# Kernel optimization log

Measured on AMD Instinct MI355X. Metric: run time of the kernel, lower is better.

## Reference

```python
import jax, jax.numpy as jnp
import numpy as np

B, IN_DIM, MEM = 8192, 4096, 256
MIN_TS, MAX_TS, EPS = 0.1, 10.0, 1e-6
LN_EPS = 1e-5


def setup_inputs() -> dict:
    key = jax.random.key(0)
    ks = jax.random.split(key, 10)
    std = 0.02
    d_in = MEM + IN_DIM  # 4352
    return {
        "x": jax.random.normal(ks[0], (B, IN_DIM), jnp.float32),
        "h": jax.random.normal(ks[1], (B, MEM), jnp.float32),
        # memory_target: Linear(d_in, 2*MEM) -> LN -> GELU -> Linear(2*MEM, MEM)
        "W1": std * jax.random.normal(ks[2], (d_in, 2 * MEM), jnp.float32),
        "b1": jnp.zeros((2 * MEM,), jnp.float32),
        "g1": jnp.ones((2 * MEM,), jnp.float32),
        "be1": jnp.zeros((2 * MEM,), jnp.float32),
        "W2": std * jax.random.normal(ks[3], (2 * MEM, MEM), jnp.float32),
        "b2": jnp.zeros((MEM,), jnp.float32),
        # decay_gate: Linear(d_in, MEM) -> sigmoid
        "Wd": std * jax.random.normal(ks[4], (d_in, MEM), jnp.float32),
        "bd": jnp.zeros((MEM,), jnp.float32),
        # input_gate: Linear(d_in, MEM) -> sigmoid
        "Wu": std * jax.random.normal(ks[5], (d_in, MEM), jnp.float32),
        "bu": jnp.zeros((MEM,), jnp.float32),
    }


def _layernorm(t, g, b):
    mu = jnp.mean(t, axis=-1, keepdims=True)
    var = jnp.mean(jnp.square(t - mu), axis=-1, keepdims=True)
    return (t - mu) * jax.lax.rsqrt(var + LN_EPS) * g + b


def reference(x, h, W1, b1, g1, be1, W2, b2, Wd, bd, Wu, bu):
    combined = jnp.concatenate([h, x], axis=-1)  # [B, MEM+IN_DIM]
    # memory_target branch: Linear -> LayerNorm -> GELU (exact) -> Linear -> tanh
    t = _layernorm(combined @ W1 + b1, g1, be1)
    t = jax.nn.gelu(t, approximate=False)
    h_candidate = jnp.tanh(t @ W2 + b2)  # [B, MEM]
    # gates
    decay = jax.nn.sigmoid(combined @ Wd + bd)
    update = jax.nn.sigmoid(combined @ Wu + bu)
    decay = MIN_TS + (MAX_TS - MIN_TS) * decay + EPS
    new_h = (1.0 - update) * (h / decay) + update * h_candidate
    # normalize_memory: rescale new_h to old h's L2 norm
    h_norm = jnp.maximum(jnp.linalg.norm(h, axis=-1, keepdims=True), EPS)
    nh_norm = jnp.maximum(jnp.linalg.norm(new_h, axis=-1, keepdims=True), 1e-12)
    new_h = new_h / nh_norm * h_norm
    return new_h
```

## Files before the change

kernel.cpp:

```cpp
#include <hip/hip_runtime.h>
#include <stdint.h>

typedef unsigned short u16;

#define B_ROWS 8192
#define IN_DIM 4096
#define MEM 256
#define D_IN 4352
#define N1 1024
#define K2 512
#define LN_EPS 1e-5f

typedef __attribute__((ext_vector_type(4))) float f32x4;
typedef __attribute__((ext_vector_type(4))) uint32_t u32x4;
typedef __attribute__((ext_vector_type(4))) unsigned short u16x4;
typedef __attribute__((ext_vector_type(8))) short bf16x8;

#define AS1(p) ((__attribute__((address_space(1))) void*)(p))
#define AS3(p) ((__attribute__((address_space(3))) void*)(p))

__device__ __forceinline__ float bf2f(u16 u) {
  union { uint32_t u; float f; } c; c.u = ((uint32_t)u) << 16; return c.f;
}
__device__ __forceinline__ u16 f2bf(float f) {
  union { float f; uint32_t u; } c; c.f = f;
  uint32_t r = (c.u + 0x7fffu + ((c.u >> 16) & 1u)) >> 16;
  return (u16)r;
}
__device__ __forceinline__ uint32_t fbits(float f) {
  union { float f; uint32_t u; } c; c.f = f; return c.u;
}
__device__ __forceinline__ uint32_t pack_trunc(float a, float b) {
  return (fbits(b) & 0xFFFF0000u) | (fbits(a) >> 16);
}

__global__ __launch_bounds__(256)
void transpose_cast_fused(const float* __restrict__ W1, const float* __restrict__ Wd,
                          const float* __restrict__ Wu, u16* __restrict__ WT) {
  __shared__ u16 tile[64][68];
  int n0 = blockIdx.x * 64, k0 = blockIdx.y * 64;
  const float* src; int srcN, ns0;
  if (n0 < 512)      { src = W1; srcN = 512; ns0 = n0; }
  else if (n0 < 768) { src = Wd; srcN = 256; ns0 = n0 - 512; }
  else               { src = Wu; srcN = 256; ns0 = n0 - 768; }
  int t = threadIdx.x;
  int rr = t >> 4;
  int c4 = (t & 15) * 4;
#pragma unroll
  for (int i = 0; i < 4; i++) {
    int k = i * 16 + rr;
    f32x4 v = *(const f32x4*)&src[(size_t)(k0 + k) * srcN + ns0 + c4];
    tile[c4 + 0][k] = f2bf(v[0]);
    tile[c4 + 1][k] = f2bf(v[1]);
    tile[c4 + 2][k] = f2bf(v[2]);
    tile[c4 + 3][k] = f2bf(v[3]);
  }
  __syncthreads();
#pragma unroll
  for (int i = 0; i < 4; i++) {
    int n = i * 16 + rr;
    u16x4 w;
    w.x = tile[n][c4 + 0];
    w.y = tile[n][c4 + 1];
    w.z = tile[n][c4 + 2];
    w.w = tile[n][c4 + 3];
    *(u16x4*)&WT[(size_t)(n0 + n) * D_IN + k0 + c4] = w;
  }
}

__global__ void transpose_cast(const float* __restrict__ src, u16* __restrict__ dst,
                               int K, int N) {
  __shared__ u16 tile[32][34];
  int n0 = blockIdx.x * 32, k0 = blockIdx.y * 32;
  int tx = threadIdx.x, ty = threadIdx.y;
#pragma unroll
  for (int i = 0; i < 4; i++)
    tile[ty + i * 8][tx] = f2bf(src[(size_t)(k0 + ty + i * 8) * N + n0 + tx]);
  __syncthreads();
#pragma unroll
  for (int i = 0; i < 4; i++)
    dst[(size_t)(n0 + ty + i * 8) * K + k0 + tx] = tile[tx][ty + i * 8];
}

__global__ __launch_bounds__(256, 4)
void gemm1_kernel(const float* __restrict__ x, const float* __restrict__ h,
                  const u16* __restrict__ WT, u16* __restrict__ G0,
                  u16* __restrict__ G1, int klen) {
  __shared__ __attribute__((aligned(16))) u16 As[128 * 64];
  __shared__ __attribute__((aligned(16))) u16 Bs[128 * 64];
  const int t = threadIdx.x;
  const int lane = t & 63, wave = t >> 6;
  const int by = blockIdx.x & 63;
  const int bx = (blockIdx.x >> 6) & 7;
  const int part = blockIdx.x >> 9;
  const int kbase = part * klen;
  u16* __restrict__ Gout = part ? G1 : G0;
  const int row0 = by * 128, col0 = bx * 128;
  const int q = lane >> 4, mrow = lane & 15;
  const int wm = wave >> 1, wn = wave & 1;

  int ar[4], ac[4];
#pragma unroll
  for (int j = 0; j < 4; j++) {
    int idx = j * 256 + t;
    int r = idx >> 3;
    ar[j] = r;
    ac[j] = (idx & 7) ^ (r & 7);
  }

  f32x4 acc[4][4] = {};

  for (int k0 = kbase; k0 < kbase + klen; k0 += 64) {
#pragma unroll
    for (int j = 0; j < 4; j++) {
      const u16* gp = WT + (size_t)(col0 + ar[j]) * D_IN + k0 + ac[j] * 8;
      __builtin_amdgcn_global_load_lds(AS1(gp), AS3(&Bs[(j * 256 + t) * 8]), 16, 0, 0);
    }
#pragma unroll
    for (int j = 0; j < 4; j++) {
      int k = k0 + ac[j] * 8;
      const float* gp = (k < MEM) ? (h + (size_t)(row0 + ar[j]) * MEM + k)
                                  : (x + (size_t)(row0 + ar[j]) * IN_DIM + (k - MEM));
      f32x4 v0 = *(const f32x4*)gp;
      f32x4 v1 = *(const f32x4*)(gp + 4);
      u32x4 w;
      w.x = pack_trunc(v0[0], v0[1]);
      w.y = pack_trunc(v0[2], v0[3]);
      w.z = pack_trunc(v1[0], v1[1]);
      w.w = pack_trunc(v1[2], v1[3]);
      *(u32x4*)&As[(j * 256 + t) * 8] = w;
    }
    __syncthreads();
#pragma unroll
    for (int kk = 0; kk < 2; kk++) {
      bf16x8 a[4], b[4];
#pragma unroll
      for (int mt = 0; mt < 4; mt++) {
        int row = wm * 64 + mt * 16 + mrow;
        int p = (kk * 4 + q) ^ (mrow & 7);
        a[mt] = *(const bf16x8*)&As[row * 64 + p * 8];
      }
#pragma unroll
      for (int nt = 0; nt < 4; nt++) {
        int row = wn * 64 + nt * 16 + mrow;
        int p = (kk * 4 + q) ^ (mrow & 7);
        b[nt] = *(const bf16x8*)&Bs[row * 64 + p * 8];
      }
#pragma unroll
      for (int mt = 0; mt < 4; mt++) {
#pragma unroll
        for (int nt = 0; nt < 4; nt++) {
          acc[mt][nt] = __builtin_amdgcn_mfma_f32_16x16x32_bf16(a[mt], b[nt], acc[mt][nt], 0, 0, 0);
        }
      }
    }
    __syncthreads();
  }
#pragma unroll
  for (int mt = 0; mt < 4; mt++) {
#pragma unroll
    for (int nt = 0; nt < 4; nt++) {
#pragma unroll
      for (int i = 0; i < 4; i++) {
        int row = row0 + wm * 64 + mt * 16 + q * 4 + i;
        int col = col0 + wn * 64 + nt * 16 + mrow;
        Gout[(size_t)row * N1 + col] = f2bf(acc[mt][nt][i]);
      }
    }
  }
}

__global__ __launch_bounds__(256)
void ln_gelu_kernel(u16* __restrict__ G0, const u16* __restrict__ G1,
                    const float* __restrict__ b1, const float* __restrict__ g1,
                    const float* __restrict__ be1, int nparts) {
  int r = blockIdx.x;
  int t = threadIdx.x;
  u16* row = G0 + (size_t)r * N1;
  uint32_t w = *(const uint32_t*)&row[2 * t];
  float z0 = bf2f((u16)(w & 0xffff));
  float z1 = bf2f((u16)(w >> 16));
  if (nparts == 2) {
    uint32_t w1 = *(const uint32_t*)&G1[(size_t)r * N1 + 2 * t];
    z0 += bf2f((u16)(w1 & 0xffff));
    z1 += bf2f((u16)(w1 >> 16));
  }
  z0 += b1[2 * t];
  z1 += b1[2 * t + 1];
  float s = z0 + z1, ss = z0 * z0 + z1 * z1;
#pragma unroll
  for (int m = 32; m >= 1; m >>= 1) {
    s += __shfl_xor(s, m, 64);
    ss += __shfl_xor(ss, m, 64);
  }
  __shared__ float rs[4], rss[4];
  int lane = t & 63, wave = t >> 6;
  if (lane == 0) { rs[wave] = s; rss[wave] = ss; }
  __syncthreads();
  float S = rs[0] + rs[1] + rs[2] + rs[3];
  float SS = rss[0] + rss[1] + rss[2] + rss[3];
  float mu = S * (1.0f / 512.0f);
  float var = SS * (1.0f / 512.0f) - mu * mu;
  float rstd = rsqrtf(var + LN_EPS);
  float y0 = (z0 - mu) * rstd * g1[2 * t] + be1[2 * t];
  float y1 = (z1 - mu) * rstd * g1[2 * t + 1] + be1[2 * t + 1];
  float o0 = 0.5f * y0 * (1.0f + erff(y0 * 0.7071067811865475f));
  float o1 = 0.5f * y1 * (1.0f + erff(y1 * 0.7071067811865475f));
  *(uint32_t*)&row[2 * t] = ((uint32_t)f2bf(o1) << 16) | f2bf(o0);
}

__global__ __launch_bounds__(256, 2)
void gemm2_epi_kernel(const u16* __restrict__ G0, const u16* __restrict__ G1,
                      const u16* __restrict__ W2T, const float* __restrict__ h,
                      const float* __restrict__ b2, const float* __restrict__ bd,
                      const float* __restrict__ bu, float* __restrict__ out,
                      int nparts) {
  __shared__ __attribute__((aligned(16))) u16 As[32 * 64];
  __shared__ __attribute__((aligned(16))) u16 Bs[256 * 64];
  __shared__ float red_nh[32][4], red_h[32][4], scl[32];
  const int t = threadIdx.x, lane = t & 63, wave = t >> 6;
  const int q = lane >> 4, mrow = lane & 15;
  const int r0 = blockIdx.x * 32;

  const int arA = t >> 3;
  const int acA = (t & 7) ^ (arA & 7);
  int brB[8], bcB[8];
#pragma unroll
  for (int j = 0; j < 8; j++) {
    int idx = j * 256 + t;
    brB[j] = idx >> 3;
    bcB[j] = (idx & 7) ^ (brB[j] & 7);
  }
  f32x4 acc[2][4] = {};
  for (int k0 = 0; k0 < K2; k0 += 64) {
    __builtin_amdgcn_global_load_lds(AS1(G0 + (size_t)(r0 + arA) * N1 + k0 + acA * 8),
                                     AS3(&As[t * 8]), 16, 0, 0);
#pragma unroll
    for (int j = 0; j < 8; j++) {
      __builtin_amdgcn_global_load_lds(AS1(W2T + (size_t)brB[j] * K2 + k0 + bcB[j] * 8),
                                       AS3(&Bs[(j * 256 + t) * 8]), 16, 0, 0);
    }
    __syncthreads();
#pragma unroll
    for (int kk = 0; kk < 2; kk++) {
      bf16x8 a[2], b[4];
#pragma unroll
      for (int mt = 0; mt < 2; mt++) {
        int row = mt * 16 + mrow;
        int p = (kk * 4 + q) ^ (row & 7);
        a[mt] = *(const bf16x8*)&As[row * 64 + p * 8];
      }
#pragma unroll
      for (int nt = 0; nt < 4; nt++) {
        int row = wave * 64 + nt * 16 + mrow;
        int p = (kk * 4 + q) ^ (row & 7);
        b[nt] = *(const bf16x8*)&Bs[row * 64 + p * 8];
      }
#pragma unroll
      for (int mt = 0; mt < 2; mt++) {
#pragma unroll
        for (int nt = 0; nt < 4; nt++) {
          acc[mt][nt] = __builtin_amdgcn_mfma_f32_16x16x32_bf16(a[mt], b[nt], acc[mt][nt], 0, 0, 0);
        }
      }
    }
    __syncthreads();
  }
  float snh[2][4], shh[2][4];
#pragma unroll
  for (int mt = 0; mt < 2; mt++) {
#pragma unroll
    for (int i = 0; i < 4; i++) {
      int r = mt * 16 + q * 4 + i;
      size_t grow = (size_t)(r0 + r);
      float a_nh = 0.f, a_h = 0.f;
#pragma unroll
      for (int nt = 0; nt < 4; nt++) {
        int c = wave * 64 + nt * 16 + mrow;
        float hc = tanhf(acc[mt][nt][i] + b2[c]);
        float zd = bf2f(G0[grow * N1 + 512 + c]);
        float zu = bf2f(G0[grow * N1 + 768 + c]);
        if (nparts == 2) {
          zd += bf2f(G1[grow * N1 + 512 + c]);
          zu += bf2f(G1[grow * N1 + 768 + c]);
        }
        zd += bd[c];
        zu += bu[c];
        float dec = 0.1f + 9.9f / (1.0f + expf(-zd)) + 1e-6f;
        float u = 1.0f / (1.0f + expf(-zu));
        float hv = h[grow * MEM + c];
        float nh = (1.0f - u) * (hv / dec) + u * hc;
        acc[mt][nt][i] = nh;
        a_nh += nh * nh;
        a_h += hv * hv;
      }
      snh[mt][i] = a_nh;
      shh[mt][i] = a_h;
    }
  }
#pragma unroll
  for (int m = 1; m <= 8; m <<= 1) {
#pragma unroll
    for (int mt = 0; mt < 2; mt++) {
#pragma unroll
      for (int i = 0; i < 4; i++) {
        snh[mt][i] += __shfl_xor(snh[mt][i], m, 64);
        shh[mt][i] += __shfl_xor(shh[mt][i], m, 64);
      }
    }
  }
  if (mrow == 0) {
#pragma unroll
    for (int mt = 0; mt < 2; mt++) {
#pragma unroll
      for (int i = 0; i < 4; i++) {
        int r = mt * 16 + q * 4 + i;
        red_nh[r][wave] = snh[mt][i];
        red_h[r][wave] = shh[mt][i];
      }
    }
  }
  __syncthreads();
  if (t < 32) {
    float tn = red_nh[t][0] + red_nh[t][1] + red_nh[t][2] + red_nh[t][3];
    float th = red_h[t][0] + red_h[t][1] + red_h[t][2] + red_h[t][3];
    float hn = fmaxf(sqrtf(th), 1e-6f);
    float nn = fmaxf(sqrtf(tn), 1e-12f);
    scl[t] = hn / nn;
  }
  __syncthreads();
#pragma unroll
  for (int mt = 0; mt < 2; mt++) {
#pragma unroll
    for (int i = 0; i < 4; i++) {
      int r = mt * 16 + q * 4 + i;
      size_t grow = (size_t)(r0 + r);
      float sc = scl[r];
#pragma unroll
      for (int nt = 0; nt < 4; nt++) {
        int c = wave * 64 + nt * 16 + mrow;
        out[grow * MEM + c] = acc[mt][nt][i] * sc;
      }
    }
  }
}

extern "C" void kernel_launch(void* const* d_in, const int* in_sizes, int n_in,
                              void* d_out, int out_size, void* d_ws, size_t ws_size,
                              hipStream_t stream) {
  const float* x   = (const float*)d_in[0];
  const float* h   = (const float*)d_in[1];
  const float* W1  = (const float*)d_in[2];
  const float* b1  = (const float*)d_in[3];
  const float* g1  = (const float*)d_in[4];
  const float* be1 = (const float*)d_in[5];
  const float* W2  = (const float*)d_in[6];
  const float* b2  = (const float*)d_in[7];
  const float* Wd  = (const float*)d_in[8];
  const float* bd  = (const float*)d_in[9];
  const float* Wu  = (const float*)d_in[10];
  const float* bu  = (const float*)d_in[11];
  float* out = (float*)d_out;

  char* ws = (char*)d_ws;
  u16* WT  = (u16*)(ws);
  u16* W2T = (u16*)(ws + 8912896);
  u16* G0  = (u16*)(ws + 9175040);
  u16* G1  = (u16*)(ws + 25952256);

  const int nparts = (ws_size >= 42729472u) ? 2 : 1;
  const int klen = D_IN / nparts;

  transpose_cast_fused<<<dim3(N1 / 64, D_IN / 64), 256, 0, stream>>>(W1, Wd, Wu, WT);
  transpose_cast<<<dim3(256 / 32, 512 / 32), dim3(32, 8), 0, stream>>>(W2, W2T, 512, 256);

  gemm1_kernel<<<512 * nparts, 256, 0, stream>>>(x, h, WT, G0, G1, klen);
  ln_gelu_kernel<<<B_ROWS, 256, 0, stream>>>(G0, G1, b1, g1, be1, nparts);
  gemm2_epi_kernel<<<B_ROWS / 32, 256, 0, stream>>>(G0, G1, W2T, h, b2, bd, bu, out, nparts);
}
```

Baseline: 388.1 us.

## Fuse LayerNorm+GELU into GEMM2 and pre-cast activations to bf16 for GEMM1

Removes the separate LayerNorm/GELU kernel. Its work moves into the prologue of the second GEMM, which now keeps 16 normalized rows in LDS, cutting one round trip of the intermediate through global memory. When the workspace is large enough, it also adds a separate pass that casts x and h to bf16 once with round-to-nearest-even. The first GEMM can then load A tiles asynchronously straight into LDS instead of converting fp32 in its inner loop. The trade-offs are an extra kernel and an extra bf16 copy of the activations, plus smaller row tiles in GEMM2 that reuse each W2 tile less.

After: 343.2 us. 1.13x faster.

```diff
diff --git a/kernel.cpp b/kernel.cpp
--- a/kernel.cpp
+++ b/kernel.cpp
@@ -30,8 +30,33 @@
 __device__ __forceinline__ uint32_t fbits(float f) {
   union { float f; uint32_t u; } c; c.f = f; return c.u;
 }
+__device__ __forceinline__ uint32_t pack_rne(float a, float b) {
+  return ((uint32_t)f2bf(b) << 16) | f2bf(a);
+}
 __device__ __forceinline__ uint32_t pack_trunc(float a, float b) {
   return (fbits(b) & 0xFFFF0000u) | (fbits(a) >> 16);
+}
+
+__global__ __launch_bounds__(256)
+void cast_A_kernel(const float* __restrict__ h, const float* __restrict__ x,
+                   u16* __restrict__ Abf) {
+  int b = blockIdx.x, t = threadIdx.x;
+  const float* src; int r, c, dcol;
+  if (b < 1024) {
+    int g = (b * 256 + t) * 8;
+    src = h + g; r = g >> 8; c = g & 255; dcol = c;
+  } else {
+    int g = ((b - 1024) * 256 + t) * 8;
+    src = x + g; r = g >> 12; c = g & 4095; dcol = MEM + c;
+  }
+  f32x4 v0 = *(const f32x4*)src;
+  f32x4 v1 = *(const f32x4*)(src + 4);
+  u32x4 w;
+  w.x = pack_rne(v0[0], v0[1]);
+  w.y = pack_rne(v0[2], v0[3]);
+  w.z = pack_rne(v1[0], v1[1]);
+  w.w = pack_rne(v1[2], v1[3]);
+  *(u32x4*)&Abf[(size_t)r * D_IN + dcol] = w;
 }
 
 __global__ __launch_bounds__(256)
@@ -83,9 +108,8 @@
 }
 
 __global__ __launch_bounds__(256, 4)
-void gemm1_kernel(const float* __restrict__ x, const float* __restrict__ h,
-                  const u16* __restrict__ WT, u16* __restrict__ G0,
-                  u16* __restrict__ G1, int klen) {
+void gemm1_pre_kernel(const u16* __restrict__ Abf, const u16* __restrict__ WT,
+                      u16* __restrict__ G0, u16* __restrict__ G1, int klen) {
   __shared__ __attribute__((aligned(16))) u16 As[128 * 64];
   __shared__ __attribute__((aligned(16))) u16 Bs[128 * 64];
   const int t = threadIdx.x;
@@ -118,6 +142,83 @@
     }
 #pragma unroll
     for (int j = 0; j < 4; j++) {
+      const u16* gp = Abf + (size_t)(row0 + ar[j]) * D_IN + k0 + ac[j] * 8;
+      __builtin_amdgcn_global_load_lds(AS1(gp), AS3(&As[(j * 256 + t) * 8]), 16, 0, 0);
+    }
+    __syncthreads();
+#pragma unroll
+    for (int kk = 0; kk < 2; kk++) {
+      bf16x8 a[4], b[4];
+#pragma unroll
+      for (int mt = 0; mt < 4; mt++) {
+        int row = wm * 64 + mt * 16 + mrow;
+        int p = (kk * 4 + q) ^ (mrow & 7);
+        a[mt] = *(const bf16x8*)&As[row * 64 + p * 8];
+      }
+#pragma unroll
+      for (int nt = 0; nt < 4; nt++) {
+        int row = wn * 64 + nt * 16 + mrow;
+        int p = (kk * 4 + q) ^ (mrow & 7);
+        b[nt] = *(const bf16x8*)&Bs[row * 64 + p * 8];
+      }
+#pragma unroll
+      for (int mt = 0; mt < 4; mt++) {
+#pragma unroll
+        for (int nt = 0; nt < 4; nt++) {
+          acc[mt][nt] = __builtin_amdgcn_mfma_f32_16x16x32_bf16(a[mt], b[nt], acc[mt][nt], 0, 0, 0);
+        }
+      }
+    }
+    __syncthreads();
+  }
+#pragma unroll
+  for (int mt = 0; mt < 4; mt++) {
+#pragma unroll
+    for (int nt = 0; nt < 4; nt++) {
+#pragma unroll
+      for (int i = 0; i < 4; i++) {
+        int row = row0 + wm * 64 + mt * 16 + q * 4 + i;
+        int col = col0 + wn * 64 + nt * 16 + mrow;
+        Gout[(size_t)row * N1 + col] = f2bf(acc[mt][nt][i]);
+      }
+    }
+  }
+}
+
+__global__ __launch_bounds__(256, 4)
+void gemm1_inline_kernel(const float* __restrict__ x, const float* __restrict__ h,
+                         const u16* __restrict__ WT, u16* __restrict__ G0,
+                         u16* __restrict__ G1, int klen) {
+  __shared__ __attribute__((aligned(16))) u16 As[128 * 64];
+  __shared__ __attribute__((aligned(16))) u16 Bs[128 * 64];
+  const int t = threadIdx.x;
+  const int lane = t & 63, wave = t >> 6;
+  const int by = blockIdx.x & 63;
+  const int bx = (blockIdx.x >> 6) & 7;
+  const int part = blockIdx.x >> 9;
+  const int kbase = part * klen;
+  u16* __restrict__ Gout = part ? G1 : G0;
+  const int row0 = by * 128, col0 = bx * 128;
+  const int q = lane >> 4, mrow = lane & 15;
+  const int wm = wave >> 1, wn = wave & 1;
+
+  int ar[4], ac[4];
+#pragma unroll
+  for (int j = 0; j < 4; j++) {
+    int idx = j * 256 + t;
+    int r = idx >> 3;
+    ar[j] = r;
+    ac[j] = (idx & 7) ^ (r & 7);
+  }
+  f32x4 acc[4][4] = {};
+  for (int k0 = kbase; k0 < kbase + klen; k0 += 64) {
+#pragma unroll
+    for (int j = 0; j < 4; j++) {
+      const u16* gp = WT + (size_t)(col0 + ar[j]) * D_IN + k0 + ac[j] * 8;
+      __builtin_amdgcn_global_load_lds(AS1(gp), AS3(&Bs[(j * 256 + t) * 8]), 16, 0, 0);
+    }
+#pragma unroll
+    for (int j = 0; j < 4; j++) {
       int k = k0 + ac[j] * 8;
       const float* gp = (k < MEM) ? (h + (size_t)(row0 + ar[j]) * MEM + k)
                                   : (x + (size_t)(row0 + ar[j]) * IN_DIM + (k - MEM));
@@ -170,60 +271,76 @@
   }
 }
 
-__global__ __launch_bounds__(256)
-void ln_gelu_kernel(u16* __restrict__ G0, const u16* __restrict__ G1,
-                    const float* __restrict__ b1, const float* __restrict__ g1,
-                    const float* __restrict__ be1, int nparts) {
-  int r = blockIdx.x;
-  int t = threadIdx.x;
-  u16* row = G0 + (size_t)r * N1;
-  uint32_t w = *(const uint32_t*)&row[2 * t];
-  float z0 = bf2f((u16)(w & 0xffff));
-  float z1 = bf2f((u16)(w >> 16));
-  if (nparts == 2) {
-    uint32_t w1 = *(const uint32_t*)&G1[(size_t)r * N1 + 2 * t];
-    z0 += bf2f((u16)(w1 & 0xffff));
-    z1 += bf2f((u16)(w1 >> 16));
-  }
-  z0 += b1[2 * t];
-  z1 += b1[2 * t + 1];
-  float s = z0 + z1, ss = z0 * z0 + z1 * z1;
-#pragma unroll
-  for (int m = 32; m >= 1; m >>= 1) {
-    s += __shfl_xor(s, m, 64);
-    ss += __shfl_xor(ss, m, 64);
-  }
-  __shared__ float rs[4], rss[4];
-  int lane = t & 63, wave = t >> 6;
-  if (lane == 0) { rs[wave] = s; rss[wave] = ss; }
-  __syncthreads();
-  float S = rs[0] + rs[1] + rs[2] + rs[3];
-  float SS = rss[0] + rss[1] + rss[2] + rss[3];
-  float mu = S * (1.0f / 512.0f);
-  float var = SS * (1.0f / 512.0f) - mu * mu;
-  float rstd = rsqrtf(var + LN_EPS);
-  float y0 = (z0 - mu) * rstd * g1[2 * t] + be1[2 * t];
-  float y1 = (z1 - mu) * rstd * g1[2 * t + 1] + be1[2 * t + 1];
-  float o0 = 0.5f * y0 * (1.0f + erff(y0 * 0.7071067811865475f));
-  float o1 = 0.5f * y1 * (1.0f + erff(y1 * 0.7071067811865475f));
-  *(uint32_t*)&row[2 * t] = ((uint32_t)f2bf(o1) << 16) | f2bf(o0);
-}
-
 __global__ __launch_bounds__(256, 2)
-void gemm2_epi_kernel(const u16* __restrict__ G0, const u16* __restrict__ G1,
-                      const u16* __restrict__ W2T, const float* __restrict__ h,
-                      const float* __restrict__ b2, const float* __restrict__ bd,
-                      const float* __restrict__ bu, float* __restrict__ out,
-                      int nparts) {
-  __shared__ __attribute__((aligned(16))) u16 As[32 * 64];
+void fused_ln_gemm2_kernel(const u16* __restrict__ G0, const u16* __restrict__ G1,
+                           const u16* __restrict__ W2T, const float* __restrict__ h,
+                           const float* __restrict__ b1v, const float* __restrict__ g1v,
+                           const float* __restrict__ be1v, const float* __restrict__ b2,
+                           const float* __restrict__ bd, const float* __restrict__ bu,
+                           float* __restrict__ out, int nparts) {
+  __shared__ __attribute__((aligned(16))) u16 As[16 * 512];
   __shared__ __attribute__((aligned(16))) u16 Bs[256 * 64];
-  __shared__ float red_nh[32][4], red_h[32][4], scl[32];
+  __shared__ float redA[16][4], redB[16][4], scl[16];
   const int t = threadIdx.x, lane = t & 63, wave = t >> 6;
   const int q = lane >> 4, mrow = lane & 15;
-  const int r0 = blockIdx.x * 32;
-
-  const int arA = t >> 3;
-  const int acA = (t & 7) ^ (arA & 7);
+  const int r0 = blockIdx.x * 16;
+
+  {
+    const int lr = t & 15;
+    const int lc = t >> 4;
+    float z[32];
+    const u16* g0p = G0 + (size_t)(r0 + lr) * N1 + lc * 32;
+    const u16* g1p = G1 + (size_t)(r0 + lr) * N1 + lc * 32;
+    float s = 0.f, ss = 0.f;
+#pragma unroll
+    for (int j = 0; j < 4; j++) {
+      u32x4 w0 = *(const u32x4*)(g0p + j * 8);
+      u32x4 w1;
+      if (nparts == 2) w1 = *(const u32x4*)(g1p + j * 8);
+#pragma unroll
+      for (int e = 0; e < 4; e++) {
+        float lo = bf2f((u16)(w0[e] & 0xffff));
+        float hi = bf2f((u16)(w0[e] >> 16));
+        if (nparts == 2) {
+          lo += bf2f((u16)(w1[e] & 0xffff));
+          hi += bf2f((u16)(w1[e] >> 16));
+        }
+        int cb = lc * 32 + j * 8 + e * 2;
+        lo += b1v[cb];
+        hi += b1v[cb + 1];
+        z[j * 8 + e * 2] = lo;
+        z[j * 8 + e * 2 + 1] = hi;
+        s += lo + hi;
+        ss += lo * lo + hi * hi;
+      }
+    }
+    s += __shfl_xor(s, 16, 64);  s += __shfl_xor(s, 32, 64);
+    ss += __shfl_xor(ss, 16, 64); ss += __shfl_xor(ss, 32, 64);
+    if (lane < 16) { redA[lr][wave] = s; redB[lr][wave] = ss; }
+    __syncthreads();
+    float S  = redA[lr][0] + redA[lr][1] + redA[lr][2] + redA[lr][3];
+    float SS = redB[lr][0] + redB[lr][1] + redB[lr][2] + redB[lr][3];
+    float mu = S * (1.0f / 512.0f);
+    float var = SS * (1.0f / 512.0f) - mu * mu;
+    float rstd = rsqrtf(var + LN_EPS);
+#pragma unroll
+    for (int j = 0; j < 4; j++) {
+      u32x4 wpk;
+#pragma unroll
+      for (int e = 0; e < 4; e++) {
+        int cb = lc * 32 + j * 8 + e * 2;
+        float y0 = (z[j * 8 + e * 2] - mu) * rstd * g1v[cb] + be1v[cb];
+        float y1 = (z[j * 8 + e * 2 + 1] - mu) * rstd * g1v[cb + 1] + be1v[cb + 1];
+        float o0 = 0.5f * y0 * (1.0f + erff(y0 * 0.7071067811865475f));
+        float o1 = 0.5f * y1 * (1.0f + erff(y1 * 0.7071067811865475f));
+        wpk[e] = pack_rne(o0, o1);
+      }
+      int p = lc * 4 + j;
+      int ps = p ^ (lr & 7);
+      *(u32x4*)&As[lr * 512 + ps * 8] = wpk;
+    }
+  }
+
   int brB[8], bcB[8];
 #pragma unroll
   for (int j = 0; j < 8; j++) {
@@ -231,10 +348,8 @@
     brB[j] = idx >> 3;
     bcB[j] = (idx & 7) ^ (brB[j] & 7);
   }
-  f32x4 acc[2][4] = {};
+  f32x4 acc[4] = {};
   for (int k0 = 0; k0 < K2; k0 += 64) {
-    __builtin_amdgcn_global_load_lds(AS1(G0 + (size_t)(r0 + arA) * N1 + k0 + acA * 8),
-                                     AS3(&As[t * 8]), 16, 0, 0);
 #pragma unroll
     for (int j = 0; j < 8; j++) {
       __builtin_amdgcn_global_load_lds(AS1(W2T + (size_t)brB[j] * K2 + k0 + bcB[j] * 8),
@@ -243,13 +358,10 @@
     __syncthreads();
 #pragma unroll
     for (int kk = 0; kk < 2; kk++) {
-      bf16x8 a[2], b[4];
-#pragma unroll
-      for (int mt = 0; mt < 2; mt++) {
-        int row = mt * 16 + mrow;
-        int p = (kk * 4 + q) ^ (row & 7);
-        a[mt] = *(const bf16x8*)&As[row * 64 + p * 8];
-      }
+      int kw = (k0 >> 5) + kk;
+      int pa = (kw * 4 + q) ^ (mrow & 7);
+      bf16x8 a = *(const bf16x8*)&As[mrow * 512 + pa * 8];
+      bf16x8 b[4];
 #pragma unroll
       for (int nt = 0; nt < 4; nt++) {
         int row = wave * 64 + nt * 16 + mrow;
@@ -257,90 +369,76 @@
         b[nt] = *(const bf16x8*)&Bs[row * 64 + p * 8];
       }
 #pragma unroll
-      for (int mt = 0; mt < 2; mt++) {
-#pragma unroll
-        for (int nt = 0; nt < 4; nt++) {
-          acc[mt][nt] = __builtin_amdgcn_mfma_f32_16x16x32_bf16(a[mt], b[nt], acc[mt][nt], 0, 0, 0);
-        }
-      }
-    }
-    __syncthreads();
-  }
-  float snh[2][4], shh[2][4];
-#pragma unroll
-  for (int mt = 0; mt < 2; mt++) {
+      for (int nt = 0; nt < 4; nt++) {
+        acc[nt] = __builtin_amdgcn_mfma_f32_16x16x32_bf16(a, b[nt], acc[nt], 0, 0, 0);
+      }
+    }
+    __syncthreads();
+  }
+
+  float snh[4], shh[4];
+#pragma unroll
+  for (int i = 0; i < 4; i++) {
+    int r = q * 4 + i;
+    size_t grow = (size_t)(r0 + r);
+    float a_nh = 0.f, a_h = 0.f;
+#pragma unroll
+    for (int nt = 0; nt < 4; nt++) {
+      int c = wave * 64 + nt * 16 + mrow;
+      float hc = tanhf(acc[nt][i] + b2[c]);
+      float zd = bf2f(G0[grow * N1 + 512 + c]);
+      float zu = bf2f(G0[grow * N1 + 768 + c]);
+      if (nparts == 2) {
+        zd += bf2f(G1[grow * N1 + 512 + c]);
+        zu += bf2f(G1[grow * N1 + 768 + c]);
+      }
+      zd += bd[c];
+      zu += bu[c];
+      float dec = 0.1f + 9.9f / (1.0f + expf(-zd)) + 1e-6f;
+      float u = 1.0f / (1.0f + expf(-zu));
+      float hv = h[grow * MEM + c];
+      float nh = (1.0f - u) * (hv / dec) + u * hc;
+      acc[nt][i] = nh;
+      a_nh += nh * nh;
+      a_h += hv * hv;
+    }
+    snh[i] = a_nh;
+    shh[i] = a_h;
+  }
+#pragma unroll
+  for (int m = 1; m <= 8; m <<= 1) {
 #pragma unroll
     for (int i = 0; i < 4; i++) {
-      int r = mt * 16 + q * 4 + i;
-      size_t grow = (size_t)(r0 + r);
-      float a_nh = 0.f, a_h = 0.f;
-#pragma unroll
-      for (int nt = 0; nt < 4; nt++) {
-        int c = wave * 64 + nt * 16 + mrow;
-        float hc = tanhf(acc[mt][nt][i] + b2[c]);
-        float zd = bf2f(G0[grow * N1 + 512 + c]);
-        float zu = bf2f(G0[grow * N1 + 768 + c]);
-        if (nparts == 2) {
-          zd += bf2f(G1[grow * N1 + 512 + c]);
-          zu += bf2f(G1[grow * N1 + 768 + c]);
-        }
-        zd += bd[c];
-        zu += bu[c];
-        float dec = 0.1f + 9.9f / (1.0f + expf(-zd)) + 1e-6f;
-        float u = 1.0f / (1.0f + expf(-zu));
-        float hv = h[grow * MEM + c];
-        float nh = (1.0f - u) * (hv / dec) + u * hc;
-        acc[mt][nt][i] = nh;
-        a_nh += nh * nh;
-        a_h += hv * hv;
-      }
-      snh[mt][i] = a_nh;
-      shh[mt][i] = a_h;
-    }
-  }
-#pragma unroll
-  for (int m = 1; m <= 8; m <<= 1) {
-#pragma unroll
-    for (int mt = 0; mt < 2; mt++) {
-#pragma unroll
-      for (int i = 0; i < 4; i++) {
-        snh[mt][i] += __shfl_xor(snh[mt][i], m, 64);
-        shh[mt][i] += __shfl_xor(shh[mt][i], m, 64);
-      }
+      snh[i] += __shfl_xor(snh[i], m, 64);
+      shh[i] += __shfl_xor(shh[i], m, 64);
     }
   }
   if (mrow == 0) {
 #pragma unroll
-    for (int mt = 0; mt < 2; mt++) {
-#pragma unroll
-      for (int i = 0; i < 4; i++) {
-        int r = mt * 16 + q * 4 + i;
-        red_nh[r][wave] = snh[mt][i];
-        red_h[r][wave] = shh[mt][i];
-      }
+    for (int i = 0; i < 4; i++) {
+      int r = q * 4 + i;
+      redA[r][wave] = snh[i];
+      redB[r][wave] = shh[i];
     }
   }
   __syncthreads();
-  if (t < 32) {
-    float tn = red_nh[t][0] + red_nh[t][1] + red_nh[t][2] + red_nh[t][3];
-    float th = red_h[t][0] + red_h[t][1] + red_h[t][2] + red_h[t][3];
+  if (t < 16) {
+    float tn = redA[t][0] + redA[t][1] + redA[t][2] + redA[t][3];
+    float th = redB[t][0] + redB[t][1] + redB[t][2] + redB[t][3];
     float hn = fmaxf(sqrtf(th), 1e-6f);
     float nn = fmaxf(sqrtf(tn), 1e-12f);
     scl[t] = hn / nn;
   }
   __syncthreads();
 #pragma unroll
-  for (int mt = 0; mt < 2; mt++) {
-#pragma unroll
-    for (int i = 0; i < 4; i++) {
-      int r = mt * 16 + q * 4 + i;
-      size_t grow = (size_t)(r0 + r);
-      float sc = scl[r];
-#pragma unroll
-      for (int nt = 0; nt < 4; nt++) {
-        int c = wave * 64 + nt * 16 + mrow;
-        out[grow * MEM + c] = acc[mt][nt][i] * sc;
-      }
+  for (int i = 0; i < 4; i++) {
+    int r = q * 4 + i;
+    size_t grow = (size_t)(r0 + r);
+    float sc = scl[r];
+#pragma unroll
+    for (int nt = 0; nt < 4; nt++) {
+      int c = wave * 64 + nt * 16 + mrow;
+      out[grow * MEM + c] = acc[nt][i] * sc;
     }
   }
 }
@@ -367,14 +465,22 @@
   u16* W2T = (u16*)(ws + 8912896);
   u16* G0  = (u16*)(ws + 9175040);
   u16* G1  = (u16*)(ws + 25952256);
+  u16* Abf = (u16*)(ws + 42729472);
 
   const int nparts = (ws_size >= 42729472u) ? 2 : 1;
   const int klen = D_IN / nparts;
+  const bool use_pre = (ws_size >= 114032640u);
 
   transpose_cast_fused<<<dim3(N1 / 64, D_IN / 64), 256, 0, stream>>>(W1, Wd, Wu, WT);
   transpose_cast<<<dim3(256 / 32, 512 / 32), dim3(32, 8), 0, stream>>>(W2, W2T, 512, 256);
 
-  gemm1_kernel<<<512 * nparts, 256, 0, stream>>>(x, h, WT, G0, G1, klen);
-  ln_gelu_kernel<<<B_ROWS, 256, 0, stream>>>(G0, G1, b1, g1, be1, nparts);
-  gemm2_epi_kernel<<<B_ROWS / 32, 256, 0, stream>>>(G0, G1, W2T, h, b2, bd, bu, out, nparts);
-}
+  if (use_pre) {
+    cast_A_kernel<<<17408, 256, 0, stream>>>(h, x, Abf);
+    gemm1_pre_kernel<<<512 * nparts, 256, 0, stream>>>(Abf, WT, G0, G1, klen);
+  } else {
+    gemm1_inline_kernel<<<512 * nparts, 256, 0, stream>>>(x, h, WT, G0, G1, klen);
+  }
+
+  fused_ln_gemm2_kernel<<<B_ROWS / 16, 256, 0, stream>>>(G0, G1, W2T, h, b1, g1, be1,
+                                                         b2, bd, bu, out, nparts);
+}
```
